# Optimization experiments

Hardware: AMD Instinct MI355X
Metric: run time of the kernel (lower is better)

The kernel has to match this reference:

```python
import jax, jax.numpy as jnp
import numpy as np

D_MODEL = 256
N_HEADS = 8
HEAD_DIM = D_MODEL // N_HEADS  # 32
B, S = 8, 2048


def setup_inputs() -> dict:
    key = jax.random.key(0)
    ks = jax.random.split(key, 8)
    scale = 1.0 / np.sqrt(D_MODEL)
    return {
        "q": jax.random.normal(ks[0], (B, S, D_MODEL), jnp.float32),
        "k": jax.random.normal(ks[1], (B, S, D_MODEL), jnp.float32),
        "v": jax.random.normal(ks[2], (B, S, D_MODEL), jnp.float32),
        # padding mask: 1.0 = masked (added as -1e9), 0.0 = keep; shape (1,1,1,S)
        "m": jax.random.randint(ks[3], (1, 1, 1, S), 0, 2).astype(jnp.float32),
        "wq": jax.random.normal(ks[4], (D_MODEL, D_MODEL), jnp.float32) * scale,
        "bq": jnp.zeros((D_MODEL,), jnp.float32),
        "wk": jax.random.normal(ks[5], (D_MODEL, D_MODEL), jnp.float32) * scale,
        "bk": jnp.zeros((D_MODEL,), jnp.float32),
        "wv": jax.random.normal(ks[6], (D_MODEL, D_MODEL), jnp.float32) * scale,
        "bv": jnp.zeros((D_MODEL,), jnp.float32),
        "wo": jax.random.normal(ks[7], (D_MODEL, D_MODEL), jnp.float32) * scale,
        "bo": jnp.zeros((D_MODEL,), jnp.float32),
    }


def _split_heads(x):
    # (B, S, D) -> (B, H, S, dh)
    b, s, _ = x.shape
    return x.reshape(b, s, N_HEADS, HEAD_DIM).transpose(0, 2, 1, 3)


def reference(q, k, v, m, wq, bq, wk, bk, wv, bv, wo, bo):
    qh = _split_heads(q @ wq + bq)
    kh = _split_heads(k @ wk + bk)
    vh = _split_heads(v @ wv + bv)
    # scaled dot-product attention with additive padding mask
    logits = jnp.einsum("bhqd,bhkd->bhqk", qh, kh) / jnp.sqrt(
        jnp.asarray(HEAD_DIM, jnp.float32)
    )
    logits = logits + m * (-1e9)
    attn = jax.nn.softmax(logits, axis=-1)
    out = jnp.einsum("bhqk,bhkd->bhqd", attn, vh)  # (B, H, S, dh)
    out = out.transpose(0, 2, 1, 3).reshape(q.shape[0], -1, D_MODEL)
    return out @ wo + bo
```

## Files before the change

### kernel.cpp

```cpp
#include <hip/hip_runtime.h>

typedef short short8 __attribute__((ext_vector_type(8)));
typedef float f32x4 __attribute__((ext_vector_type(4)));
typedef float f32x16 __attribute__((ext_vector_type(16)));
typedef unsigned int uint2v __attribute__((ext_vector_type(2)));

#define NHEADS 8
#define DHEAD 32
#define DMODEL 256
#define SEQ 2048
#define QSCALE 0.17677669529663687f
#define LOG2E 1.4426950408889634f
#define NEGBIG -1.4427e9f
#define DEFER_THR 11.0f

__device__ __forceinline__ unsigned short f2bf(float x) {
  union { float f; unsigned int u; } c; c.f = x;
  return (unsigned short)((c.u + 0x7fffu + ((c.u >> 16) & 1u)) >> 16);
}

__device__ __forceinline__ unsigned int cvtpk(float lo, float hi) {
  unsigned int r;
  asm("v_cvt_pk_bf16_f32 %0, %1, %2" : "=v"(r) : "v"(lo), "v"(hi));
  return r;
}

__device__ __forceinline__ short8 pk8(float4 a, float4 b) {
  union { unsigned int u[4]; short8 s; } r;
  r.u[0] = cvtpk(a.x, a.y);
  r.u[1] = cvtpk(a.z, a.w);
  r.u[2] = cvtpk(b.x, b.y);
  r.u[3] = cvtpk(b.z, b.w);
  return r.s;
}

__device__ __forceinline__ float fexp2(float x) {
#if __has_builtin(__builtin_amdgcn_exp2f)
  return __builtin_amdgcn_exp2f(x);
#else
  return exp2f(x);
#endif
}

__device__ __forceinline__ uint2v plswap(unsigned int a, unsigned int b) {
#if __has_builtin(__builtin_amdgcn_permlane32_swap)
  return __builtin_amdgcn_permlane32_swap(a, b, false, false);
#else
  uint2v r;
  unsigned int sa = __shfl_xor(a, 32), sb = __shfl_xor(b, 32);
  int hi = (threadIdx.x & 63) >> 5;
  r[0] = hi ? sb : a;
  r[1] = hi ? b : sa;
  return r;
#endif
}

__device__ __forceinline__ int swz(int row, int c) {
  return row * 512 + ((c ^ (row & 7)) << 4);
}

__global__ __launch_bounds__(256) void prep_scan_kernel(
    const float* __restrict__ wq, const float* __restrict__ wk,
    const float* __restrict__ wv, const float* __restrict__ wo,
    const float* __restrict__ bq, const float* __restrict__ m,
    unsigned short* __restrict__ wt, float* __restrict__ bqs,
    int* __restrict__ cidx, float* __restrict__ tailbias, int* __restrict__ nkp)
{
  __shared__ float tile[256][17];
  __shared__ int ssum[256];
  const int blk = blockIdx.x;
  const int t = threadIdx.x;
  if (blk < 64) {
    const int mi = blk >> 4, nt = blk & 15;
    const float* w = (mi == 0) ? wq : (mi == 1) ? wk : (mi == 2) ? wv : wo;
    const float scale = (mi == 0) ? QSCALE * LOG2E : 1.0f;
    {
      const float* src = w + (size_t)t * DMODEL + nt * 16;
      #pragma unroll
      for (int i = 0; i < 16; i += 4) {
        float4 f = *(const float4*)(src + i);
        tile[t][i + 0] = f.x; tile[t][i + 1] = f.y;
        tile[t][i + 2] = f.z; tile[t][i + 3] = f.w;
      }
    }
    __syncthreads();
    unsigned short* dst = wt + mi * 65536 + nt * 4096;
    #pragma unroll
    for (int gi = 0; gi < 2; gi++) {
      const int g = t * 2 + gi;
      const int kk = g >> 6, l = g & 63;
      const int fr = l & 15, hi4 = l >> 4;
      union { unsigned short us[8]; uint4 u; } o;
      #pragma unroll
      for (int j = 0; j < 8; j++)
        o.us[j] = f2bf(tile[kk * 32 + hi4 * 8 + j][fr] * scale);
      *(uint4*)(dst + g * 8) = o.u;
    }
    if (blk == 0) bqs[t] = bq[t] * QSCALE * LOG2E;
  } else {
    float mv[8];
    float4 m0 = *(const float4*)(m + t * 8);
    float4 m1 = *(const float4*)(m + t * 8 + 4);
    mv[0]=m0.x; mv[1]=m0.y; mv[2]=m0.z; mv[3]=m0.w;
    mv[4]=m1.x; mv[5]=m1.y; mv[6]=m1.z; mv[7]=m1.w;
    int keep[8], cnt = 0;
    #pragma unroll
    for (int j = 0; j < 8; j++) { keep[j] = (mv[j] == 0.0f); cnt += keep[j]; }
    ssum[t] = cnt;
    __syncthreads();
    for (int off = 1; off < 256; off <<= 1) {
      int add = (t >= off) ? ssum[t - off] : 0;
      __syncthreads();
      ssum[t] += add;
      __syncthreads();
    }
    int base = ssum[t] - cnt;
    const int nk = ssum[255];
    #pragma unroll
    for (int j = 0; j < 8; j++) {
      cidx[t * 8 + j] = keep[j] ? base : -1;
      base += keep[j];
    }
    if (t == 0) nkp[0] = nk;
    if (t < 32) {
      int g = (nk & ~31) + t;
      tailbias[t] = (g < nk) ? 0.0f : NEGBIG;
    }
  }
}

__global__ __launch_bounds__(256) void qkv_kernel(
    const float* __restrict__ q, const float* __restrict__ k,
    const float* __restrict__ v, const unsigned short* __restrict__ wt,
    const float* __restrict__ bqs, const float* __restrict__ bk,
    const float* __restrict__ bv, const int* __restrict__ cidx,
    unsigned short* __restrict__ qf, unsigned short* __restrict__ kf,
    unsigned short* __restrict__ vf)
{
  __shared__ __align__(16) char alds[16384];
  const int z = blockIdx.y;
  const int tile = blockIdx.x;
  const int t = threadIdx.x;
  const int w = t >> 6, lane = t & 63;
  const int fr = lane & 15, hi4 = lane >> 4;

  const float* x = (z == 0) ? q : (z == 1) ? k : v;
  const float* xbase = x + (size_t)tile * 32 * DMODEL;

  #pragma unroll
  for (int i = 0; i < 4; i++) {
    const int gi = i * 256 + t;
    const int row = gi >> 5, c = gi & 31;
    const float4* src = (const float4*)(xbase + row * DMODEL + c * 8);
    float4 a0 = src[0], a1 = src[1];
    *(short8*)(alds + swz(row, c)) = pk8(a0, a1);
  }
  __syncthreads();

  f32x4 acc[2][4];
  #pragma unroll
  for (int mi = 0; mi < 2; mi++)
    #pragma unroll
    for (int ni = 0; ni < 4; ni++) { acc[mi][ni][0]=0.f; acc[mi][ni][1]=0.f; acc[mi][ni][2]=0.f; acc[mi][ni][3]=0.f; }

  const unsigned short* wz = wt + z * 65536 + (w * 4) * 4096;
  for (int kk = 0; kk < DMODEL; kk += 32) {
    short8 a[2], b[4];
    #pragma unroll
    for (int mi = 0; mi < 2; mi++)
      a[mi] = *(const short8*)(alds + swz(mi * 16 + fr, (kk >> 3) + hi4));
    #pragma unroll
    for (int ni = 0; ni < 4; ni++)
      b[ni] = *(const short8*)(wz + ni * 4096 + (kk >> 5) * 512 + lane * 8);
    if (z < 2) {
      #pragma unroll
      for (int mi = 0; mi < 2; mi++)
        #pragma unroll
        for (int ni = 0; ni < 4; ni++)
          acc[mi][ni] = __builtin_amdgcn_mfma_f32_16x16x32_bf16(b[ni], a[mi], acc[mi][ni], 0, 0, 0);
    } else {
      #pragma unroll
      for (int mi = 0; mi < 2; mi++)
        #pragma unroll
        for (int ni = 0; ni < 4; ni++)
          acc[mi][ni] = __builtin_amdgcn_mfma_f32_16x16x32_bf16(a[mi], b[ni], acc[mi][ni], 0, 0, 0);
    }
  }

  if (z < 2) {
    const float* bias = (z == 0) ? bqs : bk;
    unsigned short* dstbuf = (z == 0) ? qf : kf;
    float4 bias4[4];
    #pragma unroll
    for (int ni = 0; ni < 4; ni++)
      bias4[ni] = *(const float4*)(bias + w * 64 + ni * 16 + hi4 * 4);
    #pragma unroll
    for (int mi = 0; mi < 2; mi++) {
      const int tok = tile * 32 + mi * 16 + fr;
      const int b_ = tok >> 11, sl = tok & 2047;
      const int cs = (z == 0) ? sl : cidx[sl];
      if (cs >= 0) {
        #pragma unroll
        for (int ni = 0; ni < 4; ni++) {
          const int f0 = w * 64 + ni * 16 + hi4 * 4;
          const int h = f0 >> 5, dq = f0 & 31;
          uint2 val;
          val.x = cvtpk(acc[mi][ni][0] + bias4[ni].x, acc[mi][ni][1] + bias4[ni].y);
          val.y = cvtpk(acc[mi][ni][2] + bias4[ni].z, acc[mi][ni][3] + bias4[ni].w);
          const size_t off = (size_t)(b_ * NHEADS + h) * 65536
                           + (cs >> 5) * 1024 + ((dq >> 4) & 1) * 512 + ((dq >> 3) & 1) * 256
                           + (cs & 31) * 8 + (dq & 7);
          *(uint2*)(dstbuf + off) = val;
        }
      }
    }
  } else {
    #pragma unroll
    for (int ni = 0; ni < 4; ni++) {
      const int f = w * 64 + ni * 16 + fr;
      const float bb = bv[f];
      const int h = f >> 5, d = f & 31;
      #pragma unroll
      for (int mi = 0; mi < 2; mi++) {
        #pragma unroll
        for (int j = 0; j < 4; j++) {
          const int token = tile * 32 + mi * 16 + hi4 * 4 + j;
          const int b_ = token >> 11, s = token & 2047;
          const int cs = cidx[s];
          if (cs >= 0) {
            vf[(size_t)(b_ * NHEADS + h) * 65536
               + (cs >> 5) * 1024 + ((cs >> 4) & 1) * 512 + ((cs >> 3) & 1) * 256
               + d * 8 + (cs & 7)] = f2bf(acc[mi][ni][j] + bb);
          }
        }
      }
    }
  }
}

template<bool MASKED>
__device__ __forceinline__ void attn_tile(
    short8 kf0, short8 kf1, short8 vf0, short8 vf1, short8 onesf,
    short8 q0, short8 q1, const float* __restrict__ tailbias,
    int hi, f32x16& oacc, f32x16& lacc, float& mrun)
{
  f32x16 sacc;
  #pragma unroll
  for (int i = 0; i < 16; i++) sacc[i] = -mrun;
  __builtin_amdgcn_s_setprio(1);
  sacc = __builtin_amdgcn_mfma_f32_32x32x16_bf16(kf0, q0, sacc, 0, 0, 0);
  sacc = __builtin_amdgcn_mfma_f32_32x32x16_bf16(kf1, q1, sacc, 0, 0, 0);
  __builtin_amdgcn_s_setprio(0);

  float p[16];
  if (MASKED) {
    const float4 t0 = *(const float4*)(tailbias + 4 * hi);
    const float4 t1 = *(const float4*)(tailbias + 4 * hi + 8);
    const float4 t2 = *(const float4*)(tailbias + 4 * hi + 16);
    const float4 t3 = *(const float4*)(tailbias + 4 * hi + 24);
    p[0]=sacc[0]+t0.x;  p[1]=sacc[1]+t0.y;  p[2]=sacc[2]+t0.z;  p[3]=sacc[3]+t0.w;
    p[4]=sacc[4]+t1.x;  p[5]=sacc[5]+t1.y;  p[6]=sacc[6]+t1.z;  p[7]=sacc[7]+t1.w;
    p[8]=sacc[8]+t2.x;  p[9]=sacc[9]+t2.y;  p[10]=sacc[10]+t2.z; p[11]=sacc[11]+t2.w;
    p[12]=sacc[12]+t3.x; p[13]=sacc[13]+t3.y; p[14]=sacc[14]+t3.z; p[15]=sacc[15]+t3.w;
  } else {
    #pragma unroll
    for (int i = 0; i < 16; i++) p[i] = sacc[i];
  }

  float x0 = fmaxf(fmaxf(p[0], p[1]), p[2]);
  float x1 = fmaxf(fmaxf(p[3], p[4]), p[5]);
  float x2 = fmaxf(fmaxf(p[6], p[7]), p[8]);
  float x3 = fmaxf(fmaxf(p[9], p[10]), p[11]);
  float x4 = fmaxf(fmaxf(p[12], p[13]), p[14]);
  float tmax = fmaxf(fmaxf(fmaxf(x0, x1), fmaxf(x2, x3)), fmaxf(x4, p[15]));

  if (!__all(tmax <= DEFER_THR)) {
    float pm = fmaxf(tmax, __shfl_xor(tmax, 32));
    float delta = fmaxf(pm, 0.0f);
    float corr = fexp2(-delta);
    mrun += delta;
    lacc[0] *= corr;
    #pragma unroll
    for (int i = 0; i < 16; i++) oacc[i] *= corr;
    #pragma unroll
    for (int i = 0; i < 16; i++) p[i] -= delta;
  }

  #pragma unroll
  for (int i = 0; i < 16; i++) p[i] = fexp2(p[i]);

  const unsigned int A0 = cvtpk(p[0], p[1]);
  const unsigned int A1 = cvtpk(p[2], p[3]);
  const unsigned int B0 = cvtpk(p[4], p[5]);
  const unsigned int B1 = cvtpk(p[6], p[7]);
  const unsigned int A2 = cvtpk(p[8], p[9]);
  const unsigned int A3 = cvtpk(p[10], p[11]);
  const unsigned int B2 = cvtpk(p[12], p[13]);
  const unsigned int B3 = cvtpk(p[14], p[15]);
  union { unsigned int u[4]; short8 s; } pb0, pb1;
  uint2v r0 = plswap(A0, B0); pb0.u[0] = r0[0]; pb0.u[2] = r0[1];
  uint2v r1 = plswap(A1, B1); pb0.u[1] = r1[0]; pb0.u[3] = r1[1];
  uint2v r2 = plswap(A2, B2); pb1.u[0] = r2[0]; pb1.u[2] = r2[1];
  uint2v r3 = plswap(A3, B3); pb1.u[1] = r3[0]; pb1.u[3] = r3[1];

  __builtin_amdgcn_s_setprio(1);
  lacc = __builtin_amdgcn_mfma_f32_32x32x16_bf16(onesf, pb0.s, lacc, 0, 0, 0);
  lacc = __builtin_amdgcn_mfma_f32_32x32x16_bf16(onesf, pb1.s, lacc, 0, 0, 0);
  oacc = __builtin_amdgcn_mfma_f32_32x32x16_bf16(vf0, pb0.s, oacc, 0, 0, 0);
  oacc = __builtin_amdgcn_mfma_f32_32x32x16_bf16(vf1, pb1.s, oacc, 0, 0, 0);
  __builtin_amdgcn_s_setprio(0);
}

__global__ __launch_bounds__(128) void attn_kernel(
    const unsigned short* __restrict__ qf, const unsigned short* __restrict__ kfr,
    const unsigned short* __restrict__ vfr, const float* __restrict__ tailbias,
    const int* __restrict__ nkp, unsigned short* __restrict__ attno)
{
  const int bid = blockIdx.x;
  const int L = (bid & 7) * 256 + (bid >> 3);
  const int bh = L >> 5, qt = L & 31;
  const int w = threadIdx.x >> 6, lane = threadIdx.x & 63;
  const int ql = lane & 31, hi = lane >> 5;
  const int qrow = qt * 64 + w * 32 + ql;
  const int loff = hi * 256 + ql * 8;
  const unsigned short* Qb = qf + (size_t)bh * 65536 + (size_t)(qt * 2 + w) * 1024 + loff;
  const unsigned short* Kl = kfr + (size_t)bh * 65536 + loff;
  const unsigned short* Vl = vfr + (size_t)bh * 65536 + loff;

  const short8 q0 = *(const short8*)(Qb);
  const short8 q1 = *(const short8*)(Qb + 512);

  short8 onesf;
  #pragma unroll
  for (int i = 0; i < 8; i++) onesf[i] = (short)0x3F80;

  f32x16 oacc, lacc;
  #pragma unroll
  for (int i = 0; i < 16; i++) { oacc[i] = 0.0f; lacc[i] = 0.0f; }
  float mrun = 0.0f;

  const int nk = *nkp;
  const int nfull = nk >> 5, ntail = nk & 31;
  const int ntiles = nfull + (ntail ? 1 : 0);
  const int last = (ntiles > 0) ? (ntiles - 1) : 0;

  short8 ak0 = *(const short8*)(Kl);
  short8 ak1 = *(const short8*)(Kl + 512);
  short8 av0 = *(const short8*)(Vl);
  short8 av1 = *(const short8*)(Vl + 512);
  const int nb1 = ((1 <= last) ? 1 : last) * 1024;
  short8 bk0 = *(const short8*)(Kl + nb1);
  short8 bk1 = *(const short8*)(Kl + nb1 + 512);
  short8 bv0 = *(const short8*)(Vl + nb1);
  short8 bv1 = *(const short8*)(Vl + nb1 + 512);

  int ti = 0;
  while (ti + 2 <= nfull) {
    attn_tile<false>(ak0, ak1, av0, av1, onesf, q0, q1, tailbias, hi, oacc, lacc, mrun);
    {
      const int nt = (ti + 2 <= last) ? (ti + 2) : last;
      const int nb = nt * 1024;
      ak0 = *(const short8*)(Kl + nb);
      ak1 = *(const short8*)(Kl + nb + 512);
      av0 = *(const short8*)(Vl + nb);
      av1 = *(const short8*)(Vl + nb + 512);
    }
    attn_tile<false>(bk0, bk1, bv0, bv1, onesf, q0, q1, tailbias, hi, oacc, lacc, mrun);
    {
      const int nt = (ti + 3 <= last) ? (ti + 3) : last;
      const int nb = nt * 1024;
      bk0 = *(const short8*)(Kl + nb);
      bk1 = *(const short8*)(Kl + nb + 512);
      bv0 = *(const short8*)(Vl + nb);
      bv1 = *(const short8*)(Vl + nb + 512);
    }
    ti += 2;
  }
  if (ti < nfull) {
    attn_tile<false>(ak0, ak1, av0, av1, onesf, q0, q1, tailbias, hi, oacc, lacc, mrun);
    if (ntail)
      attn_tile<true>(bk0, bk1, bv0, bv1, onesf, q0, q1, tailbias, hi, oacc, lacc, mrun);
  } else if (ntail) {
    attn_tile<true>(ak0, ak1, av0, av1, onesf, q0, q1, tailbias, hi, oacc, lacc, mrun);
  }

  const float den = lacc[0];
  const float inv = (den > 0.0f) ? (1.0f / den) : 0.0f;
  const int b = bh >> 3, h = bh & 7;
  unsigned short* orow = attno + ((size_t)(b * SEQ + qrow)) * DMODEL + h * DHEAD + 4 * hi;
  #pragma unroll
  for (int g = 0; g < 4; g++) {
    union { unsigned short us[4]; uint2 u2; } st;
    st.us[0] = f2bf(oacc[4 * g + 0] * inv);
    st.us[1] = f2bf(oacc[4 * g + 1] * inv);
    st.us[2] = f2bf(oacc[4 * g + 2] * inv);
    st.us[3] = f2bf(oacc[4 * g + 3] * inv);
    *(uint2*)(orow + 8 * g) = st.u2;
  }
}

__global__ __launch_bounds__(256) void oproj_kernel(
    const unsigned short* __restrict__ attno, const unsigned short* __restrict__ wto,
    const float* __restrict__ bo, float* __restrict__ out)
{
  __shared__ __align__(16) char alds[8192];
  const int tile = blockIdx.x;
  const int t = threadIdx.x;
  const int w = t >> 6, lane = t & 63;
  const int fr = lane & 15, hi4 = lane >> 4;
  const unsigned short* abase = attno + (size_t)tile * 16 * DMODEL;

  #pragma unroll
  for (int i = 0; i < 2; i++) {
    const int gi = i * 256 + t;
    const int row = gi >> 5, c = gi & 31;
    uint4 u = *(const uint4*)(abase + row * DMODEL + c * 8);
    *(uint4*)(alds + swz(row, c)) = u;
  }
  __syncthreads();

  f32x4 acc[4];
  #pragma unroll
  for (int ni = 0; ni < 4; ni++) { acc[ni][0]=0.f; acc[ni][1]=0.f; acc[ni][2]=0.f; acc[ni][3]=0.f; }

  const unsigned short* wz = wto + (w * 4) * 4096;
  for (int kk = 0; kk < DMODEL; kk += 32) {
    short8 a = *(const short8*)(alds + swz(fr, (kk >> 3) + hi4));
    short8 b[4];
    #pragma unroll
    for (int ni = 0; ni < 4; ni++)
      b[ni] = *(const short8*)(wz + ni * 4096 + (kk >> 5) * 512 + lane * 8);
    #pragma unroll
    for (int ni = 0; ni < 4; ni++)
      acc[ni] = __builtin_amdgcn_mfma_f32_16x16x32_bf16(a, b[ni], acc[ni], 0, 0, 0);
  }

  #pragma unroll
  for (int ni = 0; ni < 4; ni++) {
    const int f = w * 64 + ni * 16 + fr;
    const float bb = bo[f];
    #pragma unroll
    for (int j = 0; j < 4; j++) {
      const int token = tile * 16 + hi4 * 4 + j;
      out[(size_t)token * DMODEL + f] = acc[ni][j] + bb;
    }
  }
}

extern "C" void kernel_launch(void* const* d_in, const int* in_sizes, int n_in,
                              void* d_out, int out_size, void* d_ws, size_t ws_size,
                              hipStream_t stream) {
  const float* q  = (const float*)d_in[0];
  const float* k  = (const float*)d_in[1];
  const float* v  = (const float*)d_in[2];
  const float* m  = (const float*)d_in[3];
  const float* wq = (const float*)d_in[4];
  const float* bq = (const float*)d_in[5];
  const float* wk = (const float*)d_in[6];
  const float* bk = (const float*)d_in[7];
  const float* wv = (const float*)d_in[8];
  const float* bv = (const float*)d_in[9];
  const float* wo = (const float*)d_in[10];
  const float* bo = (const float*)d_in[11];
  float* out = (float*)d_out;

  char* ws = (char*)d_ws;
  unsigned short* wt    = (unsigned short*)ws;
  float* bqs            = (float*)(ws + 524288);
  float* tailbias       = (float*)(ws + 525312);
  int*   nkp            = (int*)(ws + 525440);
  int*   cidx           = (int*)(ws + 526336);
  unsigned short* qf    = (unsigned short*)(ws + 1048576);
  unsigned short* kfr   = qf + 4194304;
  unsigned short* vfr   = kfr + 4194304;
  unsigned short* attno = vfr + 4194304;

  prep_scan_kernel<<<dim3(65), dim3(256), 0, stream>>>(wq, wk, wv, wo, bq, m, wt, bqs, cidx, tailbias, nkp);
  qkv_kernel<<<dim3(512, 3), dim3(256), 0, stream>>>(q, k, v, wt, bqs, bk, bv, cidx, qf, kfr, vfr);
  attn_kernel<<<dim3(2048), dim3(128), 0, stream>>>(qf, kfr, vfr, tailbias, nkp, attno);
  oproj_kernel<<<dim3(1024), dim3(256), 0, stream>>>(attno, wt + 3 * 65536, bo, out);
}
```

Before: 176.6 us.

## Split attention KV range across two blocks and merge partials in output projection

Each attention block now covers 128 query rows with 4 waves and handles only half of the compacted key tiles. Each block writes unnormalized bf16 partial outputs plus per-row denominators to separate buffers. The output-projection kernel sums the two partials, normalizes them and converts to bf16 while staging into LDS. This split-K scheme shortens each block's serial key loop. The prefetch changes from two-stage double buffering to a single-tile lookahead. The combine only works because the running max is effectively fixed (mrun starts at 0 and rescaling is deferred), so both halves share the same scale; it also adds extra global traffic for the second partial buffer.

```diff
diff --git a/kernel.cpp b/kernel.cpp
--- a/kernel.cpp
+++ b/kernel.cpp
@@ -17,6 +17,11 @@
 __device__ __forceinline__ unsigned short f2bf(float x) {
   union { float f; unsigned int u; } c; c.f = x;
   return (unsigned short)((c.u + 0x7fffu + ((c.u >> 16) & 1u)) >> 16);
+}
+
+__device__ __forceinline__ float bf2f(unsigned short s) {
+  union { unsigned int u; float f; } c; c.u = ((unsigned int)s) << 16;
+  return c.f;
 }
 
 __device__ __forceinline__ unsigned int cvtpk(float lo, float hi) {
@@ -311,19 +316,20 @@
   __builtin_amdgcn_s_setprio(0);
 }
 
-__global__ __launch_bounds__(128) void attn_kernel(
+__global__ __launch_bounds__(256) void attn_kernel(
     const unsigned short* __restrict__ qf, const unsigned short* __restrict__ kfr,
     const unsigned short* __restrict__ vfr, const float* __restrict__ tailbias,
-    const int* __restrict__ nkp, unsigned short* __restrict__ attno)
+    const int* __restrict__ nkp, unsigned short* __restrict__ po0,
+    unsigned short* __restrict__ po1, float* __restrict__ pl)
 {
   const int bid = blockIdx.x;
   const int L = (bid & 7) * 256 + (bid >> 3);
-  const int bh = L >> 5, qt = L & 31;
+  const int bh = L >> 5, qt = (L >> 1) & 15, sp = L & 1;
   const int w = threadIdx.x >> 6, lane = threadIdx.x & 63;
   const int ql = lane & 31, hi = lane >> 5;
-  const int qrow = qt * 64 + w * 32 + ql;
+  const int qrow = qt * 128 + w * 32 + ql;
   const int loff = hi * 256 + ql * 8;
-  const unsigned short* Qb = qf + (size_t)bh * 65536 + (size_t)(qt * 2 + w) * 1024 + loff;
+  const unsigned short* Qb = qf + (size_t)bh * 65536 + (size_t)(qt * 4 + w) * 1024 + loff;
   const unsigned short* Kl = kfr + (size_t)bh * 65536 + loff;
   const unsigned short* Vl = vfr + (size_t)bh * 65536 + loff;
 
@@ -342,65 +348,47 @@
   const int nk = *nkp;
   const int nfull = nk >> 5, ntail = nk & 31;
   const int ntiles = nfull + (ntail ? 1 : 0);
-  const int last = (ntiles > 0) ? (ntiles - 1) : 0;
-
-  short8 ak0 = *(const short8*)(Kl);
-  short8 ak1 = *(const short8*)(Kl + 512);
-  short8 av0 = *(const short8*)(Vl);
-  short8 av1 = *(const short8*)(Vl + 512);
-  const int nb1 = ((1 <= last) ? 1 : last) * 1024;
-  short8 bk0 = *(const short8*)(Kl + nb1);
-  short8 bk1 = *(const short8*)(Kl + nb1 + 512);
-  short8 bv0 = *(const short8*)(Vl + nb1);
-  short8 bv1 = *(const short8*)(Vl + nb1 + 512);
-
-  int ti = 0;
-  while (ti + 2 <= nfull) {
-    attn_tile<false>(ak0, ak1, av0, av1, onesf, q0, q1, tailbias, hi, oacc, lacc, mrun);
-    {
-      const int nt = (ti + 2 <= last) ? (ti + 2) : last;
-      const int nb = nt * 1024;
-      ak0 = *(const short8*)(Kl + nb);
-      ak1 = *(const short8*)(Kl + nb + 512);
-      av0 = *(const short8*)(Vl + nb);
-      av1 = *(const short8*)(Vl + nb + 512);
-    }
-    attn_tile<false>(bk0, bk1, bv0, bv1, onesf, q0, q1, tailbias, hi, oacc, lacc, mrun);
-    {
-      const int nt = (ti + 3 <= last) ? (ti + 3) : last;
-      const int nb = nt * 1024;
-      bk0 = *(const short8*)(Kl + nb);
-      bk1 = *(const short8*)(Kl + nb + 512);
-      bv0 = *(const short8*)(Vl + nb);
-      bv1 = *(const short8*)(Vl + nb + 512);
-    }
-    ti += 2;
-  }
-  if (ti < nfull) {
-    attn_tile<false>(ak0, ak1, av0, av1, onesf, q0, q1, tailbias, hi, oacc, lacc, mrun);
-    if (ntail)
-      attn_tile<true>(bk0, bk1, bv0, bv1, onesf, q0, q1, tailbias, hi, oacc, lacc, mrun);
-  } else if (ntail) {
-    attn_tile<true>(ak0, ak1, av0, av1, onesf, q0, q1, tailbias, hi, oacc, lacc, mrun);
-  }
-
-  const float den = lacc[0];
-  const float inv = (den > 0.0f) ? (1.0f / den) : 0.0f;
+  const int nt0 = ntiles >> 1;
+  const int t0 = sp ? nt0 : 0;
+  const int tfe = sp ? nfull : nt0;
+  const bool dotail = (sp == 1) && (ntail != 0);
+  const int tlast = dotail ? (ntiles - 1) : (tfe - 1);
+
+  short8 ck0 = *(const short8*)(Kl + t0 * 1024);
+  short8 ck1 = *(const short8*)(Kl + t0 * 1024 + 512);
+  short8 cv0 = *(const short8*)(Vl + t0 * 1024);
+  short8 cv1 = *(const short8*)(Vl + t0 * 1024 + 512);
+
+  for (int t = t0; t < tfe; t++) {
+    const int pn = (t + 1 <= tlast) ? (t + 1) : t;
+    const int nb = pn * 1024;
+    short8 nk0 = *(const short8*)(Kl + nb);
+    short8 nk1 = *(const short8*)(Kl + nb + 512);
+    short8 nv0 = *(const short8*)(Vl + nb);
+    short8 nv1 = *(const short8*)(Vl + nb + 512);
+    attn_tile<false>(ck0, ck1, cv0, cv1, onesf, q0, q1, tailbias, hi, oacc, lacc, mrun);
+    ck0 = nk0; ck1 = nk1; cv0 = nv0; cv1 = nv1;
+  }
+  if (dotail)
+    attn_tile<true>(ck0, ck1, cv0, cv1, onesf, q0, q1, tailbias, hi, oacc, lacc, mrun);
+
+  unsigned short* posp = sp ? po1 : po0;
   const int b = bh >> 3, h = bh & 7;
-  unsigned short* orow = attno + ((size_t)(b * SEQ + qrow)) * DMODEL + h * DHEAD + 4 * hi;
+  const int row = b * SEQ + qrow;
+  unsigned short* orow = posp + (size_t)row * DMODEL + h * DHEAD + 4 * hi;
   #pragma unroll
   for (int g = 0; g < 4; g++) {
-    union { unsigned short us[4]; uint2 u2; } st;
-    st.us[0] = f2bf(oacc[4 * g + 0] * inv);
-    st.us[1] = f2bf(oacc[4 * g + 1] * inv);
-    st.us[2] = f2bf(oacc[4 * g + 2] * inv);
-    st.us[3] = f2bf(oacc[4 * g + 3] * inv);
-    *(uint2*)(orow + 8 * g) = st.u2;
-  }
+    uint2 st;
+    st.x = cvtpk(oacc[4 * g + 0], oacc[4 * g + 1]);
+    st.y = cvtpk(oacc[4 * g + 2], oacc[4 * g + 3]);
+    *(uint2*)(orow + 8 * g) = st;
+  }
+  if (hi == 0) pl[(sp << 17) + (row << 3) + h] = lacc[0];
 }
 
 __global__ __launch_bounds__(256) void oproj_kernel(
-    const unsigned short* __restrict__ attno, const unsigned short* __restrict__ wto,
+    const unsigned short* __restrict__ po0, const unsigned short* __restrict__ po1,
+    const float* __restrict__ pl, const unsigned short* __restrict__ wto,
     const float* __restrict__ bo, float* __restrict__ out)
 {
   __shared__ __align__(16) char alds[8192];
@@ -408,14 +396,27 @@
   const int t = threadIdx.x;
   const int w = t >> 6, lane = t & 63;
   const int fr = lane & 15, hi4 = lane >> 4;
-  const unsigned short* abase = attno + (size_t)tile * 16 * DMODEL;
 
   #pragma unroll
   for (int i = 0; i < 2; i++) {
     const int gi = i * 256 + t;
     const int row = gi >> 5, c = gi & 31;
-    uint4 u = *(const uint4*)(abase + row * DMODEL + c * 8);
-    *(uint4*)(alds + swz(row, c)) = u;
+    const int token = tile * 16 + row;
+    const int h = c >> 2;
+    const size_t off = (size_t)token * DMODEL + c * 8;
+    union { uint4 u; unsigned short us[8]; } a0, a1;
+    a0.u = *(const uint4*)(po0 + off);
+    a1.u = *(const uint4*)(po1 + off);
+    const float den = pl[(token << 3) + h] + pl[(1 << 17) + (token << 3) + h];
+    const float inv = (den > 0.0f) ? (1.0f / den) : 0.0f;
+    union { unsigned int u[4]; uint4 q; } o;
+    #pragma unroll
+    for (int j = 0; j < 4; j++) {
+      float flo = (bf2f(a0.us[2 * j]) + bf2f(a1.us[2 * j])) * inv;
+      float fhi = (bf2f(a0.us[2 * j + 1]) + bf2f(a1.us[2 * j + 1])) * inv;
+      o.u[j] = cvtpk(flo, fhi);
+    }
+    *(uint4*)(alds + swz(row, c)) = o.q;
   }
   __syncthreads();
 
@@ -473,10 +474,12 @@
   unsigned short* qf    = (unsigned short*)(ws + 1048576);
   unsigned short* kfr   = qf + 4194304;
   unsigned short* vfr   = kfr + 4194304;
-  unsigned short* attno = vfr + 4194304;
+  unsigned short* po0   = vfr + 4194304;
+  unsigned short* po1   = po0 + 4194304;
+  float* pl             = (float*)(po1 + 4194304);
 
   prep_scan_kernel<<<dim3(65), dim3(256), 0, stream>>>(wq, wk, wv, wo, bq, m, wt, bqs, cidx, tailbias, nkp);
   qkv_kernel<<<dim3(512, 3), dim3(256), 0, stream>>>(q, k, v, wt, bqs, bk, bv, cidx, qf, kfr, vfr);
-  attn_kernel<<<dim3(2048), dim3(128), 0, stream>>>(qf, kfr, vfr, tailbias, nkp, attno);
-  oproj_kernel<<<dim3(1024), dim3(256), 0, stream>>>(attno, wt + 3 * 65536, bo, out);
-}
+  attn_kernel<<<dim3(2048), dim3(256), 0, stream>>>(qf, kfr, vfr, tailbias, nkp, po0, po1, pl);
+  oproj_kernel<<<dim3(1024), dim3(256), 0, stream>>>(po0, po1, pl, wt + 3 * 65536, bo, out);
+}
```

Measured after the change: 173.9 us. Within noise of the previous version (-1.5%).
